# Optimization experiments

Measured on AMD Instinct MI355X. Metric: run time of the kernel, lower is better.

## Reference

```python
import jax, jax.numpy as jnp
import numpy as np

N_NODES = 50000
N_EDGES = 800000
IN_DIM = 128
HID = 128
N_GRAPHS = 64


def setup_inputs() -> dict:
    key = jax.random.key(0)
    ks = jax.random.split(key, 12)
    edge_index = jax.random.randint(ks[0], (2, N_EDGES), 0, N_NODES, dtype=jnp.int64)
    edge_weight = jax.random.uniform(ks[1], (N_EDGES,), dtype=jnp.float32)
    input_feature = jax.random.normal(ks[2], (N_NODES, IN_DIM), dtype=jnp.float32)
    graph_indicator = jnp.sort(jax.random.randint(ks[3], (N_NODES,), 0, N_GRAPHS, dtype=jnp.int64))
    s = 0.05
    W1 = jax.random.normal(ks[4], (IN_DIM, HID), dtype=jnp.float32) * s
    b1 = jnp.zeros((HID,), jnp.float32)
    W2 = jax.random.normal(ks[5], (HID, HID), dtype=jnp.float32) * s
    b2 = jnp.zeros((HID,), jnp.float32)
    W3 = jax.random.normal(ks[6], (HID, HID), dtype=jnp.float32) * s
    b3 = jnp.zeros((HID,), jnp.float32)
    wa = jax.random.normal(ks[7], (3 * HID, 1), dtype=jnp.float32) * s
    ba = jnp.zeros((1,), jnp.float32)
    Wf = jax.random.normal(ks[8], (3 * HID * 2, IN_DIM), dtype=jnp.float32) * s
    bf = jnp.zeros((IN_DIM,), jnp.float32)
    return dict(edge_index=edge_index, edge_weight=edge_weight,
                input_feature=input_feature, graph_indicator=graph_indicator,
                W1=W1, b1=b1, W2=W2, b2=b2, W3=W3, b3=b3,
                wa=wa, ba=ba, Wf=Wf, bf=bf)


def reference(edge_index, edge_weight, input_feature, graph_indicator,
              W1, b1, W2, b2, W3, b3, wa, ba, Wf, bf):
    src, dst = edge_index[0], edge_index[1]

    def gcn(x, W, b):
        # GraphConvolution: adj @ (x @ W) + b, adj given as weighted edge list
        support = x @ W  # [N, d_out]
        msg = edge_weight[:, None] * support[src]  # [E, d_out] gather
        return jax.ops.segment_sum(msg, dst, num_segments=N_NODES) + b

    g1 = jax.nn.relu(gcn(input_feature, W1, b1))
    g2 = jax.nn.relu(gcn(g1, W2, b2))
    g3 = jax.nn.relu(gcn(g2, W3, b3))
    h = jnp.concatenate([g1, g2, g3], axis=1)  # [N, 3*HID]

    # SelfAttentionPooling: attention score via a 1-dim GraphConvolution, tanh gate
    score = jnp.tanh(gcn(h, wa, ba))  # [N, 1]
    pool = h * score

    # segment avg / max pooling per graph
    seg_sum = jax.ops.segment_sum(pool, graph_indicator, num_segments=N_GRAPHS)
    counts = jax.ops.segment_sum(jnp.ones((N_NODES, 1), pool.dtype), graph_indicator,
                                 num_segments=N_GRAPHS)
    avg = seg_sum / jnp.maximum(counts, 1.0)
    mx = jax.ops.segment_max(pool, graph_indicator, num_segments=N_GRAPHS)
    pooled = jnp.concatenate([avg, mx], axis=1)  # [G, 6*HID]

    return jax.nn.relu(pooled @ Wf + bf)  # [G, IN_DIM]
```

## Files before the change

### kernel.cpp

```cpp
#include <hip/hip_runtime.h>
#include <math.h>

#define HID 128
#define POOL_SEG 16
#define WT_STRIDE 136
#define ELL_D 48
#define FXS 16384.0f
#define FXI (1.0f/16384.0f)

typedef __attribute__((ext_vector_type(8))) short short8;
typedef __attribute__((ext_vector_type(4))) float float4v;

__device__ inline short f2bf(float f) {
  unsigned u = __builtin_bit_cast(unsigned, f);
  unsigned r = (u + 0x7fff + ((u >> 16) & 1)) >> 16;
  return (short)r;
}
__device__ inline unsigned pack2bf(float lo, float hi) {
  return (unsigned)(unsigned short)f2bf(lo) | ((unsigned)(unsigned short)f2bf(hi) << 16);
}
__device__ inline float bflo(unsigned u) { return __builtin_bit_cast(float, u << 16); }
__device__ inline float bfhi(unsigned u) { return __builtin_bit_cast(float, u & 0xffff0000u); }
__device__ inline float bf2f(unsigned short s) { return __builtin_bit_cast(float, (unsigned)s << 16); }
__device__ inline unsigned short f2h(float f) {
  _Float16 h = (_Float16)f;
  return __builtin_bit_cast(unsigned short, h);
}
__device__ inline float h2f(unsigned short hb) {
  return (float)__builtin_bit_cast(_Float16, hb);
}

__global__ __launch_bounds__(256) void prologue(
    const void* __restrict__ ei_raw, const float* __restrict__ ew,
    int* __restrict__ cursor, unsigned* __restrict__ ell,
    const float* __restrict__ W1, const float* __restrict__ W2, const float* __restrict__ W3,
    short* __restrict__ T1, short* __restrict__ T2, short* __restrict__ T3,
    const void* __restrict__ gi_raw, int* __restrict__ gstart,
    int E, int N, int G, int EB) {
  int b = blockIdx.x, t = threadIdx.x;
  if (b < EB) {
    int e = b * 256 + t;
    if (e < E) {
      const int* pw = (const int*)ei_raw;
      int nz = 0;
#pragma unroll
      for (int i = 1; i < 64; i += 2) nz |= pw[i];
      int s, d;
      if (nz == 0) {
        const long long* p = (const long long*)ei_raw;
        s = (int)p[e]; d = (int)p[E + e];
      } else {
        const int* p = (const int*)ei_raw;
        s = p[e]; d = p[E + e];
      }
      unsigned short wh = f2h(ew[e]);
      int pos = atomicAdd(&cursor[d], 1);
      if (pos < ELL_D)
        ell[(size_t)d * ELL_D + pos] = ((unsigned)s << 16) | (unsigned)wh;
    }
  } else if (b < EB + 192) {
    int i = (b - EB) * 256 + t;
    int which = i >> 14, idx = i & 16383;
    int k = idx >> 7, nn = idx & 127;
    const float* W = (which == 0) ? W1 : ((which == 1) ? W2 : W3);
    short* T = (which == 0) ? T1 : ((which == 1) ? T2 : T3);
    T[nn * WT_STRIDE + k] = f2bf(W[idx]);
  } else {
    int g = t;
    if (g > G) return;
    if (g == G) { gstart[g] = N; return; }
    bool is64 = (((const int*)gi_raw)[N - 1] == 0);
    const long long* g64 = (const long long*)gi_raw;
    const int* g32 = (const int*)gi_raw;
    int lo = 0, hi = N;
    while (lo < hi) {
      int mid = (lo + hi) >> 1;
      long long v = is64 ? g64[mid] : (long long)g32[mid];
      if (v < (long long)g) lo = mid + 1; else hi = mid;
    }
    gstart[g] = lo;
  }
}

__global__ __launch_bounds__(256) void hist_k(const int* __restrict__ cursor,
                                              int* __restrict__ hist_blk, int n, int nb) {
  __shared__ int lh[ELL_D + 1];
  int t = threadIdx.x;
  if (t <= ELL_D) lh[t] = 0;
  __syncthreads();
  int i = blockIdx.x * 256 + t;
  if (i < n) {
    int d = cursor[i]; if (d > ELL_D) d = ELL_D;
    atomicAdd(&lh[d], 1);
  }
  __syncthreads();
  if (t <= ELL_D) hist_blk[t * nb + blockIdx.x] = lh[t];
}

__global__ __launch_bounds__(64) void scan_k(int* __restrict__ hist_blk, int nb) {
  __shared__ int tot[ELL_D + 1];
  __shared__ int base_s[ELL_D + 1];
  int b = threadIdx.x;
  if (b <= ELL_D) {
    int s = 0;
#pragma unroll 8
    for (int k = 0; k < nb; k++) s += hist_blk[b * nb + k];
    tot[b] = s;
  }
  __syncthreads();
  if (b == 0) {
    int r = 0;
    for (int d = 0; d <= ELL_D; d++) { base_s[d] = r; r += tot[d]; }
  }
  __syncthreads();
  if (b <= ELL_D) {
    int r = base_s[b];
#pragma unroll 8
    for (int k = 0; k < nb; k++) {
      int c = hist_blk[b * nb + k];
      hist_blk[b * nb + k] = r;
      r += c;
    }
  }
}

__global__ __launch_bounds__(256) void gemm_mfma(const float* __restrict__ Af,
                                                 const unsigned short* __restrict__ Abf,
                                                 const short* __restrict__ Wt,
                                                 unsigned short* __restrict__ C,
                                                 int n, int a_is_bf16, int gemm_nb,
                                                 const int* __restrict__ deg,
                                                 const int* __restrict__ hist_blk,
                                                 int* __restrict__ perm, int nb) {
  if (blockIdx.x >= gemm_nb) {
    int blk = blockIdx.x - gemm_nb;
    __shared__ int lcnt[ELL_D + 1];
    __shared__ int lbase[ELL_D + 1];
    int t = threadIdx.x;
    if (t <= ELL_D) {
      lcnt[t] = 0;
      lbase[t] = hist_blk[t * nb + blk];
    }
    __syncthreads();
    int idx = blk * 256 + t;
    int dg = 0, rank = 0;
    if (idx < n) {
      dg = deg[idx]; if (dg > ELL_D) dg = ELL_D;
      rank = atomicAdd(&lcnt[dg], 1);
    }
    __syncthreads();
    if (idx < n) perm[lbase[dg] + rank] = idx;
    return;
  }
  __shared__ short Wlds[128 * WT_STRIDE];
  int t = threadIdx.x;
  {
    const ulonglong2* gsrc = (const ulonglong2*)Wt;
    ulonglong2* ldst = (ulonglong2*)Wlds;
    for (int i = t; i < (128 * WT_STRIDE) / 8; i += 256) ldst[i] = gsrc[i];
  }
  __syncthreads();

  int wave = t >> 6, lane = t & 63;
  int quad = lane >> 4, l15 = lane & 15;
  int m0 = blockIdx.x * 64 + wave * 16;
  size_t SL = (size_t)n * 32;

  int m = m0 + l15; if (m >= n) m = n - 1;
  short8 afrag[4];
  if (a_is_bf16) {
#pragma unroll
    for (int c = 0; c < 4; c++)
      afrag[c] = *(const short8*)(Abf + c * SL + (size_t)m * 32 + quad * 8);
  } else {
    const float* Arow = Af + (size_t)m * 128;
#pragma unroll
    for (int c = 0; c < 4; c++) {
      int k0 = c * 32 + quad * 8;
      float4 x = *(const float4*)(Arow + k0);
      float4 y = *(const float4*)(Arow + k0 + 4);
      short8 a;
      a[0] = f2bf(x.x); a[1] = f2bf(x.y); a[2] = f2bf(x.z); a[3] = f2bf(x.w);
      a[4] = f2bf(y.x); a[5] = f2bf(y.y); a[6] = f2bf(y.z); a[7] = f2bf(y.w);
      afrag[c] = a;
    }
  }

  float4v acc[8];
#pragma unroll
  for (int tt = 0; tt < 8; tt++) acc[tt] = (float4v){0.f, 0.f, 0.f, 0.f};

#pragma unroll
  for (int c = 0; c < 4; c++) {
    int kb = c * 32 + quad * 8;
#pragma unroll
    for (int tt = 0; tt < 8; tt++) {
      const short8* bp = (const short8*)&Wlds[(tt * 16 + l15) * WT_STRIDE + kb];
      acc[tt] = __builtin_amdgcn_mfma_f32_16x16x32_bf16(afrag[c], *bp, acc[tt], 0, 0, 0);
    }
  }

  int rbase = m0 + quad * 4;
#pragma unroll
  for (int tt = 0; tt < 8; tt++) {
    int within = (tt & 1) * 16 + l15;
    size_t sb = (size_t)(tt >> 1) * SL;
#pragma unroll
    for (int r = 0; r < 4; r++) {
      int row = rbase + r;
      if (row < n) C[sb + (size_t)row * 32 + within] = (unsigned short)f2bf(acc[tt][r]);
    }
  }
}

__global__ __launch_bounds__(256) void aggregate_sl(
    const unsigned short* __restrict__ support, const int* __restrict__ deg_arr,
    const unsigned* __restrict__ ell, const float* __restrict__ bias,
    unsigned short* __restrict__ out,
    const unsigned short* __restrict__ g1p, const unsigned short* __restrict__ g2p,
    const float* __restrict__ wa, int* __restrict__ s_pre_fx,
    const int* __restrict__ perm, int n, int do_score) {
  int group = blockIdx.x & 7;
  int slice = group >> 1;
  int chunk = (blockIdx.x >> 3) * 2 + (group & 1);
  int t = threadIdx.x;
  int pos = chunk * 64 + (t >> 2);
  int q = t & 3;
  if (pos >= n) return;
  int node = perm[pos];

  int deg = deg_arr[node]; if (deg > ELL_D) deg = ELL_D;
  const unsigned* row = ell + (size_t)node * ELL_D;
  const uint4* sb = (const uint4*)support + (size_t)slice * n * 4 + q;

  int acc[8];
#pragma unroll
  for (int j = 0; j < 8; j++) acc[j] = 0;

  int i = 0;
  for (; i + 3 < deg; i += 4) {
    uint4 rr = *(const uint4*)(row + i);
    float w0 = h2f((unsigned short)(rr.x & 0xFFFF)) * FXS;
    float w1 = h2f((unsigned short)(rr.y & 0xFFFF)) * FXS;
    float w2 = h2f((unsigned short)(rr.z & 0xFFFF)) * FXS;
    float w3 = h2f((unsigned short)(rr.w & 0xFFFF)) * FXS;
    uint4 v0 = sb[(size_t)(rr.x >> 16) * 4];
    uint4 v1 = sb[(size_t)(rr.y >> 16) * 4];
    uint4 v2 = sb[(size_t)(rr.z >> 16) * 4];
    uint4 v3 = sb[(size_t)(rr.w >> 16) * 4];
    acc[0] += __float2int_rn(w0 * bflo(v0.x)); acc[1] += __float2int_rn(w0 * bfhi(v0.x));
    acc[2] += __float2int_rn(w0 * bflo(v0.y)); acc[3] += __float2int_rn(w0 * bfhi(v0.y));
    acc[4] += __float2int_rn(w0 * bflo(v0.z)); acc[5] += __float2int_rn(w0 * bfhi(v0.z));
    acc[6] += __float2int_rn(w0 * bflo(v0.w)); acc[7] += __float2int_rn(w0 * bfhi(v0.w));
    acc[0] += __float2int_rn(w1 * bflo(v1.x)); acc[1] += __float2int_rn(w1 * bfhi(v1.x));
    acc[2] += __float2int_rn(w1 * bflo(v1.y)); acc[3] += __float2int_rn(w1 * bfhi(v1.y));
    acc[4] += __float2int_rn(w1 * bflo(v1.z)); acc[5] += __float2int_rn(w1 * bfhi(v1.z));
    acc[6] += __float2int_rn(w1 * bflo(v1.w)); acc[7] += __float2int_rn(w1 * bfhi(v1.w));
    acc[0] += __float2int_rn(w2 * bflo(v2.x)); acc[1] += __float2int_rn(w2 * bfhi(v2.x));
    acc[2] += __float2int_rn(w2 * bflo(v2.y)); acc[3] += __float2int_rn(w2 * bfhi(v2.y));
    acc[4] += __float2int_rn(w2 * bflo(v2.z)); acc[5] += __float2int_rn(w2 * bfhi(v2.z));
    acc[6] += __float2int_rn(w2 * bflo(v2.w)); acc[7] += __float2int_rn(w2 * bfhi(v2.w));
    acc[0] += __float2int_rn(w3 * bflo(v3.x)); acc[1] += __float2int_rn(w3 * bfhi(v3.x));
    acc[2] += __float2int_rn(w3 * bflo(v3.y)); acc[3] += __float2int_rn(w3 * bfhi(v3.y));
    acc[4] += __float2int_rn(w3 * bflo(v3.z)); acc[5] += __float2int_rn(w3 * bfhi(v3.z));
    acc[6] += __float2int_rn(w3 * bflo(v3.w)); acc[7] += __float2int_rn(w3 * bfhi(v3.w));
  }
  for (; i < deg; i++) {
    unsigned r0 = row[i];
    float w0 = h2f((unsigned short)(r0 & 0xFFFF)) * FXS;
    uint4 v0 = sb[(size_t)(r0 >> 16) * 4];
    acc[0] += __float2int_rn(w0 * bflo(v0.x)); acc[1] += __float2int_rn(w0 * bfhi(v0.x));
    acc[2] += __float2int_rn(w0 * bflo(v0.y)); acc[3] += __float2int_rn(w0 * bfhi(v0.y));
    acc[4] += __float2int_rn(w0 * bflo(v0.z)); acc[5] += __float2int_rn(w0 * bfhi(v0.z));
    acc[6] += __float2int_rn(w0 * bflo(v0.w)); acc[7] += __float2int_rn(w0 * bfhi(v0.w));
  }

  float f[8];
#pragma unroll
  for (int j = 0; j < 8; j++) f[j] = (float)acc[j] * FXI;

  float4 b0 = ((const float4*)bias)[slice * 8 + q * 2];
  float4 b1 = ((const float4*)bias)[slice * 8 + q * 2 + 1];
  f[0] = fmaxf(f[0] + b0.x, 0.f); f[1] = fmaxf(f[1] + b0.y, 0.f);
  f[2] = fmaxf(f[2] + b0.z, 0.f); f[3] = fmaxf(f[3] + b0.w, 0.f);
  f[4] = fmaxf(f[4] + b1.x, 0.f); f[5] = fmaxf(f[5] + b1.y, 0.f);
  f[6] = fmaxf(f[6] + b1.z, 0.f); f[7] = fmaxf(f[7] + b1.w, 0.f);

  uint4 o;
  o.x = pack2bf(f[0], f[1]); o.y = pack2bf(f[2], f[3]);
  o.z = pack2bf(f[4], f[5]); o.w = pack2bf(f[6], f[7]);
  ((uint4*)out)[(size_t)slice * n * 4 + (size_t)node * 4 + q] = o;

  if (do_score) {
    uint4 u1 = ((const uint4*)g1p)[(size_t)slice * n * 4 + (size_t)node * 4 + q];
    uint4 u2 = ((const uint4*)g2p)[(size_t)slice * n * 4 + (size_t)node * 4 + q];
    const float* wa1 = wa + slice * 32 + q * 8;
    const float* wa2 = wa1 + 128;
    const float* wa3 = wa1 + 256;
    float sc = bflo(u1.x) * wa1[0] + bfhi(u1.x) * wa1[1]
             + bflo(u1.y) * wa1[2] + bfhi(u1.y) * wa1[3]
             + bflo(u1.z) * wa1[4] + bfhi(u1.z) * wa1[5]
             + bflo(u1.w) * wa1[6] + bfhi(u1.w) * wa1[7]
             + bflo(u2.x) * wa2[0] + bfhi(u2.x) * wa2[1]
             + bflo(u2.y) * wa2[2] + bfhi(u2.y) * wa2[3]
             + bflo(u2.z) * wa2[4] + bfhi(u2.z) * wa2[5]
             + bflo(u2.w) * wa2[6] + bfhi(u2.w) * wa2[7];
#pragma unroll
    for (int j = 0; j < 8; j++) sc += f[j] * wa3[j];
    sc += __shfl_xor(sc, 1, 64);
    sc += __shfl_xor(sc, 2, 64);
    if (q == 0) atomicAdd(&s_pre_fx[node], __float2int_rn(sc * FXS));
  }
}

__global__ __launch_bounds__(384) void pool_partial(const unsigned short* __restrict__ g1,
                                                    const unsigned short* __restrict__ g2,
                                                    const unsigned short* __restrict__ g3,
                                                    const int* __restrict__ s_pre_fx,
                                                    const int* __restrict__ deg_arr,
                                                    const unsigned* __restrict__ ell,
                                                    const float* __restrict__ ba,
                                                    const int* __restrict__ gstart,
                                                    float* __restrict__ part, int n) {
  int g = blockIdx.x / POOL_SEG, seg = blockIdx.x % POOL_SEG;
  int t = threadIdx.x;
  int sg = t >> 7, dd = t & 127;
  const unsigned short* gp = (sg == 0) ? g1 : ((sg == 1) ? g2 : g3);
  const unsigned short* col = gp + (size_t)(dd >> 5) * ((size_t)n * 32) + (dd & 31);
  int s = gstart[g], e = gstart[g + 1];
  int len = e - s;
  int chunk = (len + POOL_SEG - 1) / POOL_SEG;
  int ns = s + seg * chunk;
  int ne = ns + chunk; if (ne > e) ne = e;
  float ba0 = ba[0];
  __shared__ float sc_lds[256];
  float sum = 0.f, mx = -3.402823466e38f;
  for (int tb = ns; tb < ne; tb += 256) {
    int te = tb + 256; if (te > ne) te = ne;
    __syncthreads();
    if (t < te - tb) {
      int node = tb + t;
      int deg = deg_arr[node]; if (deg > ELL_D) deg = ELL_D;
      const unsigned* row = ell + (size_t)node * ELL_D;
      int acc = 0;
      for (int i = 0; i < deg; i++) {
        unsigned r = row[i];
        acc += __float2int_rn(h2f((unsigned short)(r & 0xFFFF)) * (float)s_pre_fx[r >> 16]);
      }
      sc_lds[t] = tanhf((float)acc * FXI + ba0);
    }
    __syncthreads();
    for (int node = tb; node < te; node++) {
      float v = bf2f(col[(size_t)node * 32]) * sc_lds[node - tb];
      sum += v;
      mx = fmaxf(mx, v);
    }
  }
  size_t base = (size_t)blockIdx.x * 768;
  part[base + t] = sum;
  part[base + 384 + t] = mx;
}

__global__ __launch_bounds__(512) void tail(const float* __restrict__ part,
                                            const int* __restrict__ gstart,
                                            const float* __restrict__ Wf,
                                            const float* __restrict__ bfb,
                                            float* __restrict__ out) {
  __shared__ float pooled[768];
  __shared__ float red[512];
  int g = blockIdx.x, t = threadIdx.x;
  float cnt = (float)(gstart[g + 1] - gstart[g]);
  float inv = 1.0f / fmaxf(cnt, 1.0f);
  if (t < 384) {
    int d = t;
    float sum = 0.f, mx = -3.402823466e38f;
    for (int seg = 0; seg < POOL_SEG; seg++) {
      size_t base = ((size_t)g * POOL_SEG + seg) * 768;
      sum += part[base + d];
      mx = fmaxf(mx, part[base + 384 + d]);
    }
    pooled[d] = sum * inv;
    pooled[384 + d] = mx;
  }
  __syncthreads();
  int kc = t >> 7, c = t & 127;
  float acc = (kc == 0) ? bfb[c] : 0.f;
  int k0 = kc * 192;
#pragma unroll 8
  for (int k = k0; k < k0 + 192; k++) acc += pooled[k] * Wf[(size_t)k * 128 + c];
  red[t] = acc;
  __syncthreads();
  if (t < 128)
    out[(size_t)g * 128 + t] =
        fmaxf(red[t] + red[t + 128] + red[t + 256] + red[t + 384], 0.f);
}

extern "C" void kernel_launch(void* const* d_in, const int* in_sizes, int n_in,
                              void* d_out, int out_size, void* d_ws, size_t ws_size,
                              hipStream_t stream) {
  const void* ei_raw = d_in[0];
  const float* ew    = (const float*)d_in[1];
  const float* X     = (const float*)d_in[2];
  const void* gi_raw = d_in[3];
  const float* W1 = (const float*)d_in[4];  const float* b1 = (const float*)d_in[5];
  const float* W2 = (const float*)d_in[6];  const float* b2 = (const float*)d_in[7];
  const float* W3 = (const float*)d_in[8];  const float* b3 = (const float*)d_in[9];
  const float* wa = (const float*)d_in[10]; const float* ba = (const float*)d_in[11];
  const float* Wf = (const float*)d_in[12]; const float* bf = (const float*)d_in[13];
  float* out = (float*)d_out;

  const int E = in_sizes[1];
  const int N = in_sizes[2] / 128;
  const int G = out_size / 128;

  char* ws = (char*)d_ws;
  size_t off = 0;
  auto take = [&](size_t bytes) {
    char* p = ws + off;
    off = (off + bytes + 255) & ~(size_t)255;
    return p;
  };
  const int NB256 = (N + 255) / 256;
  int* zb = (int*)take((size_t)N * 8);
  int* cursor   = zb;
  int* s_pre_fx = zb + N;
  int* hist_blk = (int*)take((size_t)(ELL_D + 1) * NB256 * 4);
  int* perm     = (int*)take((size_t)N * 4);
  unsigned* ell = (unsigned*)take((size_t)N * ELL_D * 4);
  short*    wt1 = (short*)take((size_t)128 * WT_STRIDE * 2);
  short*    wt2 = (short*)take((size_t)128 * WT_STRIDE * 2);
  short*    wt3 = (short*)take((size_t)128 * WT_STRIDE * 2);
  unsigned short* support = (unsigned short*)take((size_t)N * 128 * 2);
  unsigned short* g1      = (unsigned short*)take((size_t)N * 128 * 2);
  unsigned short* g2      = (unsigned short*)take((size_t)N * 128 * 2);
  unsigned short* g3      = (unsigned short*)take((size_t)N * 128 * 2);
  int*   gstart  = (int*)take((size_t)(G + 1) * 4);
  float* part    = (float*)take((size_t)G * POOL_SEG * 768 * 4);
  if (off > ws_size) return;

  hipMemsetAsync(zb, 0, (size_t)N * 8, stream);

  const int EB = (E + 255) / 256;
  prologue<<<EB + 192 + 1, 256, 0, stream>>>(ei_raw, ew, cursor, ell,
                                             W1, W2, W3, wt1, wt2, wt3,
                                             gi_raw, gstart, E, N, G, EB);
  hist_k<<<NB256, 256, 0, stream>>>(cursor, hist_blk, N, NB256);
  scan_k<<<1, 64, 0, stream>>>(hist_blk, NB256);

  const int GB = (N + 63) / 64;
  const int NB64 = (N + 63) / 64;
  const int AGB = 8 * ((NB64 + 1) / 2);
  gemm_mfma<<<GB + NB256, 256, 0, stream>>>(X, (const unsigned short*)nullptr, wt1,
                                            support, N, 0, GB, cursor, hist_blk, perm, NB256);
  aggregate_sl<<<AGB, 256, 0, stream>>>(support, cursor, ell, b1, g1,
                                        nullptr, nullptr, nullptr, nullptr, perm, N, 0);
  gemm_mfma<<<GB, 256, 0, stream>>>((const float*)nullptr, g1, wt2, support, N, 1, GB,
                                    nullptr, nullptr, nullptr, 0);
  aggregate_sl<<<AGB, 256, 0, stream>>>(support, cursor, ell, b2, g2,
                                        nullptr, nullptr, nullptr, nullptr, perm, N, 0);
  gemm_mfma<<<GB, 256, 0, stream>>>((const float*)nullptr, g2, wt3, support, N, 1, GB,
                                    nullptr, nullptr, nullptr, 0);
  aggregate_sl<<<AGB, 256, 0, stream>>>(support, cursor, ell, b3, g3,
                                        g1, g2, wa, s_pre_fx, perm, N, 1);

  pool_partial<<<G * POOL_SEG, 384, 0, stream>>>(g1, g2, g3, s_pre_fx, cursor, ell,
                                                 ba, gstart, part, N);
  tail<<<G, 512, 0, stream>>>(part, gstart, Wf, bf, out);
}
```

Measured before the change: 348.8 us.

## Split ELL build into packed pass plus XCD-partitioned scatter; use float accumulators

The edge prologue now writes a packed (dst|src, weight) record per edge. A new scatter_ell kernel rereads those records, and each of 8 block groups (blockIdx & 7, presumably one per XCD) handles only one eighth of the destination range. This keeps cursor atomics and ELL writes local to one L2 slice instead of bouncing across chiplets, at the cost of an extra pass over the edges and 8x redundant reads of the packed array. Separately, the aggregation accumulators switch from int adds of rounded products to float adds of rintf products, removing float-to-int conversions but changing exactness once sums exceed 2^24.

```diff
diff --git a/kernel.cpp b/kernel.cpp
--- a/kernel.cpp
+++ b/kernel.cpp
@@ -5,6 +5,7 @@
 #define POOL_SEG 16
 #define WT_STRIDE 136
 #define ELL_D 48
+#define SC_CHUNK 2048
 #define FXS 16384.0f
 #define FXI (1.0f/16384.0f)
 
@@ -32,7 +33,7 @@
 
 __global__ __launch_bounds__(256) void prologue(
     const void* __restrict__ ei_raw, const float* __restrict__ ew,
-    int* __restrict__ cursor, unsigned* __restrict__ ell,
+    int2* __restrict__ packed,
     const float* __restrict__ W1, const float* __restrict__ W2, const float* __restrict__ W3,
     short* __restrict__ T1, short* __restrict__ T2, short* __restrict__ T3,
     const void* __restrict__ gi_raw, int* __restrict__ gstart,
@@ -53,10 +54,7 @@
         const int* p = (const int*)ei_raw;
         s = p[e]; d = p[E + e];
       }
-      unsigned short wh = f2h(ew[e]);
-      int pos = atomicAdd(&cursor[d], 1);
-      if (pos < ELL_D)
-        ell[(size_t)d * ELL_D + pos] = ((unsigned)s << 16) | (unsigned)wh;
+      packed[e] = make_int2((d << 16) | s, __builtin_bit_cast(int, ew[e]));
     }
   } else if (b < EB + 192) {
     int i = (b - EB) * 256 + t;
@@ -82,6 +80,30 @@
   }
 }
 
+__global__ void scatter_ell(const int2* __restrict__ packed, int* __restrict__ cursor,
+                            unsigned* __restrict__ ell, int E, int N) {
+  int group = blockIdx.x & 7;
+  int chunk = blockIdx.x >> 3;
+  int rng = (N + 7) >> 3;
+  int lo = group * rng;
+  int hi = lo + rng; if (hi > N) hi = N;
+  int base = chunk * SC_CHUNK;
+  for (int i = 0; i < SC_CHUNK; i += 256) {
+    int e = base + i + threadIdx.x;
+    if (e < E) {
+      int2 rec = packed[e];
+      int d = ((unsigned)rec.x) >> 16;
+      if (d >= lo && d < hi) {
+        unsigned s = (unsigned)rec.x & 0xFFFFu;
+        unsigned short wh = f2h(__builtin_bit_cast(float, rec.y));
+        int pos = atomicAdd(&cursor[d], 1);
+        if (pos < ELL_D)
+          ell[(size_t)d * ELL_D + pos] = (s << 16) | (unsigned)wh;
+      }
+    }
+  }
+}
+
 __global__ __launch_bounds__(256) void hist_k(const int* __restrict__ cursor,
                                               int* __restrict__ hist_blk, int n, int nb) {
   __shared__ int lh[ELL_D + 1];
@@ -233,9 +255,9 @@
   const unsigned* row = ell + (size_t)node * ELL_D;
   const uint4* sb = (const uint4*)support + (size_t)slice * n * 4 + q;
 
-  int acc[8];
-#pragma unroll
-  for (int j = 0; j < 8; j++) acc[j] = 0;
+  float acc[8];
+#pragma unroll
+  for (int j = 0; j < 8; j++) acc[j] = 0.f;
 
   int i = 0;
   for (; i + 3 < deg; i += 4) {
@@ -248,36 +270,36 @@
     uint4 v1 = sb[(size_t)(rr.y >> 16) * 4];
     uint4 v2 = sb[(size_t)(rr.z >> 16) * 4];
     uint4 v3 = sb[(size_t)(rr.w >> 16) * 4];
-    acc[0] += __float2int_rn(w0 * bflo(v0.x)); acc[1] += __float2int_rn(w0 * bfhi(v0.x));
-    acc[2] += __float2int_rn(w0 * bflo(v0.y)); acc[3] += __float2int_rn(w0 * bfhi(v0.y));
-    acc[4] += __float2int_rn(w0 * bflo(v0.z)); acc[5] += __float2int_rn(w0 * bfhi(v0.z));
-    acc[6] += __float2int_rn(w0 * bflo(v0.w)); acc[7] += __float2int_rn(w0 * bfhi(v0.w));
-    acc[0] += __float2int_rn(w1 * bflo(v1.x)); acc[1] += __float2int_rn(w1 * bfhi(v1.x));
-    acc[2] += __float2int_rn(w1 * bflo(v1.y)); acc[3] += __float2int_rn(w1 * bfhi(v1.y));
-    acc[4] += __float2int_rn(w1 * bflo(v1.z)); acc[5] += __float2int_rn(w1 * bfhi(v1.z));
-    acc[6] += __float2int_rn(w1 * bflo(v1.w)); acc[7] += __float2int_rn(w1 * bfhi(v1.w));
-    acc[0] += __float2int_rn(w2 * bflo(v2.x)); acc[1] += __float2int_rn(w2 * bfhi(v2.x));
-    acc[2] += __float2int_rn(w2 * bflo(v2.y)); acc[3] += __float2int_rn(w2 * bfhi(v2.y));
-    acc[4] += __float2int_rn(w2 * bflo(v2.z)); acc[5] += __float2int_rn(w2 * bfhi(v2.z));
-    acc[6] += __float2int_rn(w2 * bflo(v2.w)); acc[7] += __float2int_rn(w2 * bfhi(v2.w));
-    acc[0] += __float2int_rn(w3 * bflo(v3.x)); acc[1] += __float2int_rn(w3 * bfhi(v3.x));
-    acc[2] += __float2int_rn(w3 * bflo(v3.y)); acc[3] += __float2int_rn(w3 * bfhi(v3.y));
-    acc[4] += __float2int_rn(w3 * bflo(v3.z)); acc[5] += __float2int_rn(w3 * bfhi(v3.z));
-    acc[6] += __float2int_rn(w3 * bflo(v3.w)); acc[7] += __float2int_rn(w3 * bfhi(v3.w));
+    acc[0] += rintf(w0 * bflo(v0.x)); acc[1] += rintf(w0 * bfhi(v0.x));
+    acc[2] += rintf(w0 * bflo(v0.y)); acc[3] += rintf(w0 * bfhi(v0.y));
+    acc[4] += rintf(w0 * bflo(v0.z)); acc[5] += rintf(w0 * bfhi(v0.z));
+    acc[6] += rintf(w0 * bflo(v0.w)); acc[7] += rintf(w0 * bfhi(v0.w));
+    acc[0] += rintf(w1 * bflo(v1.x)); acc[1] += rintf(w1 * bfhi(v1.x));
+    acc[2] += rintf(w1 * bflo(v1.y)); acc[3] += rintf(w1 * bfhi(v1.y));
+    acc[4] += rintf(w1 * bflo(v1.z)); acc[5] += rintf(w1 * bfhi(v1.z));
+    acc[6] += rintf(w1 * bflo(v1.w)); acc[7] += rintf(w1 * bfhi(v1.w));
+    acc[0] += rintf(w2 * bflo(v2.x)); acc[1] += rintf(w2 * bfhi(v2.x));
+    acc[2] += rintf(w2 * bflo(v2.y)); acc[3] += rintf(w2 * bfhi(v2.y));
+    acc[4] += rintf(w2 * bflo(v2.z)); acc[5] += rintf(w2 * bfhi(v2.z));
+    acc[6] += rintf(w2 * bflo(v2.w)); acc[7] += rintf(w2 * bfhi(v2.w));
+    acc[0] += rintf(w3 * bflo(v3.x)); acc[1] += rintf(w3 * bfhi(v3.x));
+    acc[2] += rintf(w3 * bflo(v3.y)); acc[3] += rintf(w3 * bfhi(v3.y));
+    acc[4] += rintf(w3 * bflo(v3.z)); acc[5] += rintf(w3 * bfhi(v3.z));
+    acc[6] += rintf(w3 * bflo(v3.w)); acc[7] += rintf(w3 * bfhi(v3.w));
   }
   for (; i < deg; i++) {
     unsigned r0 = row[i];
     float w0 = h2f((unsigned short)(r0 & 0xFFFF)) * FXS;
     uint4 v0 = sb[(size_t)(r0 >> 16) * 4];
-    acc[0] += __float2int_rn(w0 * bflo(v0.x)); acc[1] += __float2int_rn(w0 * bfhi(v0.x));
-    acc[2] += __float2int_rn(w0 * bflo(v0.y)); acc[3] += __float2int_rn(w0 * bfhi(v0.y));
-    acc[4] += __float2int_rn(w0 * bflo(v0.z)); acc[5] += __float2int_rn(w0 * bfhi(v0.z));
-    acc[6] += __float2int_rn(w0 * bflo(v0.w)); acc[7] += __float2int_rn(w0 * bfhi(v0.w));
+    acc[0] += rintf(w0 * bflo(v0.x)); acc[1] += rintf(w0 * bfhi(v0.x));
+    acc[2] += rintf(w0 * bflo(v0.y)); acc[3] += rintf(w0 * bfhi(v0.y));
+    acc[4] += rintf(w0 * bflo(v0.z)); acc[5] += rintf(w0 * bfhi(v0.z));
+    acc[6] += rintf(w0 * bflo(v0.w)); acc[7] += rintf(w0 * bfhi(v0.w));
   }
 
   float f[8];
 #pragma unroll
-  for (int j = 0; j < 8; j++) f[j] = (float)acc[j] * FXI;
+  for (int j = 0; j < 8; j++) f[j] = acc[j] * FXI;
 
   float4 b0 = ((const float4*)bias)[slice * 8 + q * 2];
   float4 b1 = ((const float4*)bias)[slice * 8 + q * 2 + 1];
@@ -342,12 +364,12 @@
       int node = tb + t;
       int deg = deg_arr[node]; if (deg > ELL_D) deg = ELL_D;
       const unsigned* row = ell + (size_t)node * ELL_D;
-      int acc = 0;
+      float acc = 0.f;
       for (int i = 0; i < deg; i++) {
         unsigned r = row[i];
-        acc += __float2int_rn(h2f((unsigned short)(r & 0xFFFF)) * (float)s_pre_fx[r >> 16]);
+        acc += rintf(h2f((unsigned short)(r & 0xFFFF)) * (float)s_pre_fx[r >> 16]);
       }
-      sc_lds[t] = tanhf((float)acc * FXI + ba0);
+      sc_lds[t] = tanhf(acc * FXI + ba0);
     }
     __syncthreads();
     for (int node = tb; node < te; node++) {
@@ -426,6 +448,7 @@
   int* s_pre_fx = zb + N;
   int* hist_blk = (int*)take((size_t)(ELL_D + 1) * NB256 * 4);
   int* perm     = (int*)take((size_t)N * 4);
+  int2* packed  = (int2*)take((size_t)E * 8);
   unsigned* ell = (unsigned*)take((size_t)N * ELL_D * 4);
   short*    wt1 = (short*)take((size_t)128 * WT_STRIDE * 2);
   short*    wt2 = (short*)take((size_t)128 * WT_STRIDE * 2);
@@ -441,9 +464,13 @@
   hipMemsetAsync(zb, 0, (size_t)N * 8, stream);
 
   const int EB = (E + 255) / 256;
-  prologue<<<EB + 192 + 1, 256, 0, stream>>>(ei_raw, ew, cursor, ell,
+  prologue<<<EB + 192 + 1, 256, 0, stream>>>(ei_raw, ew, packed,
                                              W1, W2, W3, wt1, wt2, wt3,
                                              gi_raw, gstart, E, N, G, EB);
+  {
+    int chunks = (E + SC_CHUNK - 1) / SC_CHUNK;
+    scatter_ell<<<8 * chunks, 256, 0, stream>>>(packed, cursor, ell, E, N);
+  }
   hist_k<<<NB256, 256, 0, stream>>>(cursor, hist_blk, N, NB256);
   scan_k<<<1, 64, 0, stream>>>(hist_blk, NB256);
 
```

Measured after the change: 343.4 us. Within noise of the previous version (-1.6%).
